# Optimization experiments

Measured on AMD Instinct MI355X. Metric: run time of the kernel, lower is better.

The kernel has to match this reference:

```python
import jax, jax.numpy as jnp
import numpy as np

N, D_IN = 65536, 512
H1, H2, D_SH = 1024, 1024, 512   # shared net: num_nodes_shared = [1024, 1024, 512]
HI = 512                          # indiv hidden width, num_nodes_indiv = [512, 512]


def setup_inputs() -> dict:
    key = jax.random.key(0)
    ks = jax.random.split(key, 16)
    s = 0.02
    inp = {
        "input": jax.random.normal(ks[0], (N, D_IN), jnp.float32),
        "treatment": jax.random.randint(ks[1], (N,), 0, 2, jnp.int32),
        # shared net (hidden ReLU layers + linear output, all with bias)
        "W0": jax.random.normal(ks[2], (D_IN, H1), jnp.float32) * s,
        "b0": jnp.zeros((H1,), jnp.float32),
        "W1": jax.random.normal(ks[3], (H1, H2), jnp.float32) * s,
        "b1": jnp.zeros((H2,), jnp.float32),
        "W2": jax.random.normal(ks[4], (H2, D_SH), jnp.float32) * s,
        "b2": jnp.zeros((D_SH,), jnp.float32),
        # risk net 0 (output layer has no bias)
        "A0": jax.random.normal(ks[5], (D_SH, HI), jnp.float32) * s,
        "a0": jnp.zeros((HI,), jnp.float32),
        "A1": jax.random.normal(ks[6], (HI, HI), jnp.float32) * s,
        "a1": jnp.zeros((HI,), jnp.float32),
        "A2": jax.random.normal(ks[7], (HI, 1), jnp.float32) * s,
        # risk net 1
        "C0": jax.random.normal(ks[8], (D_SH, HI), jnp.float32) * s,
        "c0": jnp.zeros((HI,), jnp.float32),
        "C1": jax.random.normal(ks[9], (HI, HI), jnp.float32) * s,
        "c1": jnp.zeros((HI,), jnp.float32),
        "C2": jax.random.normal(ks[10], (HI, 1), jnp.float32) * s,
    }
    return inp


def _risk_net(h, U0, u0, U1, u1, U2):
    h = jax.nn.relu(h @ U0 + u0)
    h = jax.nn.relu(h @ U1 + u1)
    return h @ U2  # [N, 1], no output bias


def reference(input, treatment, W0, b0, W1, b1, W2, b2,
              A0, a0, A1, a1, A2, C0, c0, C1, c1, C2):
    # shared MLP
    h = jax.nn.relu(input @ W0 + b0)
    h = jax.nn.relu(h @ W1 + b1)
    out = h @ W2 + b2                     # [N, D_SH]
    # Binary expert routing. The torch code gathers samples per treatment,
    # runs each group through its own MLP and scatters results back; the
    # math is equivalent to applying both experts and selecting per sample.
    y0 = _risk_net(out, A0, a0, A1, a1, A2)[:, 0]  # [N]
    y1 = _risk_net(out, C0, c0, C1, c1, C2)[:, 0]  # [N]
    y = jnp.where(treatment == 0, y0, y1)          # [N]
    return (y, out)
```

## Files before the change

kernel.cpp:

```cpp
#include <hip/hip_runtime.h>
#include <hip/hip_bf16.h>
#include <stdint.h>

typedef short short8 __attribute__((ext_vector_type(8)));
typedef float f32x4 __attribute__((ext_vector_type(4)));

#define NSAMP 65536
#define AS1 __attribute__((address_space(1)))
#define AS3 __attribute__((address_space(3)))

__device__ __forceinline__ unsigned short f2bf(float f) {
    union { float f; unsigned u; } v; v.f = f;
    unsigned u = v.u;
    u += 0x7fffu + ((u >> 16) & 1u);
    return (unsigned short)(u >> 16);
}


__global__ void k_convert_bf16(const float* __restrict__ in, unsigned short* __restrict__ out, int n8) {
    int i = blockIdx.x * blockDim.x + threadIdx.x;
    if (i >= n8) return;
    const float4* p = (const float4*)in + (size_t)i * 2;
    float4 a = p[0], b = p[1];
    short8 o;
    o[0] = (short)f2bf(a.x); o[1] = (short)f2bf(a.y);
    o[2] = (short)f2bf(a.z); o[3] = (short)f2bf(a.w);
    o[4] = (short)f2bf(b.x); o[5] = (short)f2bf(b.y);
    o[6] = (short)f2bf(b.z); o[7] = (short)f2bf(b.w);
    ((short8*)out)[i] = o;
}

struct PrepArgs {
    const float *W0, *W1, *W2, *A0, *C0, *A1, *C1, *a0v, *c0v;
    unsigned short *W0T, *W1T, *W2T, *RT0, *A1T, *C1T;
    float *bcat, *y0, *y1;
};
__global__ void k_prep(PrepArgs p) {
    int i = blockIdx.x * blockDim.x + threadIdx.x;
    if (i < 524288)  { int k = i >> 10, n = i & 1023; p.W0T[n * 512 + k] = f2bf(p.W0[i]); return; }
    i -= 524288;
    if (i < 1048576) { int k = i >> 10, n = i & 1023; p.W1T[n * 1024 + k] = f2bf(p.W1[i]); return; }
    i -= 1048576;
    if (i < 524288)  { int k = i >> 9, n = i & 511; p.W2T[n * 1024 + k] = f2bf(p.W2[i]); return; }
    i -= 524288;
    if (i < 262144)  { int k = i >> 9, n = i & 511; p.RT0[n * 512 + k] = f2bf(p.A0[i]); return; }
    i -= 262144;
    if (i < 262144)  { int k = i >> 9, n = i & 511; p.RT0[(512 + n) * 512 + k] = f2bf(p.C0[i]); return; }
    i -= 262144;
    if (i < 262144)  { int k = i >> 9, n = i & 511; p.A1T[n * 512 + k] = f2bf(p.A1[i]); return; }
    i -= 262144;
    if (i < 262144)  { int k = i >> 9, n = i & 511; p.C1T[n * 512 + k] = f2bf(p.C1[i]); return; }
    i -= 262144;
    if (i < 512)     { p.bcat[i] = p.a0v[i]; return; }
    i -= 512;
    if (i < 512)     { p.bcat[512 + i] = p.c0v[i]; return; }
    i -= 512;
    if (i < 65536)   { p.y0[i] = 0.f; return; }
    i -= 65536;
    if (i < 65536)   { p.y1[i] = 0.f; return; }
}

__global__ void k_select(const float* __restrict__ y0, const float* __restrict__ y1,
                         const int* __restrict__ t, float* __restrict__ y, int n) {
    int i = blockIdx.x * blockDim.x + threadIdx.x;
    if (i < n) y[i] = (t[i] == 0) ? y0[i] : y1[i];
}

template<int MODE>
__global__ __launch_bounds__(512, 2)
void k_gemm256(const unsigned short* __restrict__ A, int lda, int colOff,
               const unsigned short* __restrict__ BT,
               const float* __restrict__ bias,
               unsigned short* __restrict__ Cbf,
               float* __restrict__ Cf32,
               const float* __restrict__ w2,
               float* __restrict__ ydot,
               int Ncols, int K, int NB)
{
    __shared__ __align__(16) char lds[131072];

    const int tid  = threadIdx.x;
    const int lane = tid & 63;
    const int wid  = tid >> 6;
    const int wr   = wid >> 2;
    const int wcn  = wid & 3;

    const int nwg = gridDim.x;
    const int bid = blockIdx.x;
    const int swz = (bid & 7) * (nwg >> 3) + (bid >> 3);
    const int mt = swz / NB, nt = swz % NB;
    const int m0 = mt << 8, n0 = nt << 8;

    const int srow = tid >> 2;
    const int scs  = (tid & 3) ^ ((srow >> 1) & 3);
    const unsigned short* gA0 = A  + (size_t)(m0 + srow) * lda + colOff + scs * 8;
    const unsigned short* gA1 = gA0 + (size_t)128 * lda;
    const unsigned short* gB0 = BT + (size_t)(n0 + srow) * K + scs * 8;
    const unsigned short* gB1 = gB0 + (size_t)128 * K;
    const int ldst = wid * 1024;

#define STAGE_BLK(dbuf, blkoff, g0, g1, koff)                                            \
    do {                                                                                 \
        __builtin_amdgcn_global_load_lds((const AS1 void*)((g0) + (koff)),               \
                                         (AS3 void*)((dbuf) + (blkoff) + ldst), 16, 0, 0); \
        __builtin_amdgcn_global_load_lds((const AS1 void*)((g1) + (koff)),               \
                                         (AS3 void*)((dbuf) + (blkoff) + 8192 + ldst), 16, 0, 0); \
    } while (0)

    int aOff[8], bOff[4];
#pragma unroll
    for (int i = 0; i < 8; ++i) {
        int r = wr * 128 + i * 16 + (lane & 15);
        aOff[i] = r * 64 + ((((lane >> 4) ^ ((r >> 1) & 3))) << 4);
    }
#pragma unroll
    for (int j = 0; j < 4; ++j) {
        int r = wcn * 64 + j * 16 + (lane & 15);
        bOff[j] = r * 64 + ((((lane >> 4) ^ ((r >> 1) & 3))) << 4);
    }

    f32x4 acc[8][4];
#pragma unroll
    for (int i = 0; i < 8; ++i)
#pragma unroll
        for (int j = 0; j < 4; ++j) acc[i][j] = (f32x4)0.f;

    const int KT = K >> 6;

    STAGE_BLK(lds, 0,     gA0, gA1, 0);
    STAGE_BLK(lds, 32768, gB0, gB1, 0);
    STAGE_BLK(lds, 16384, gA0, gA1, 32);
    STAGE_BLK(lds, 49152, gB0, gB1, 32);
    asm volatile("s_waitcnt vmcnt(4)" ::: "memory");
    __builtin_amdgcn_s_barrier();

    for (int t = 0; t < KT; ++t) {
        const char* sbuf = lds + (t & 1) * 65536;
        char* dbuf = lds + ((t + 1) & 1) * 65536;
        const int koff = ((t + 1) << 6);
        const bool st = (t + 1 < KT);
        short8 af[4], bfv[4];

#pragma unroll
        for (int i = 0; i < 4; ++i) af[i]  = *(const short8*)(sbuf + aOff[i]);
#pragma unroll
        for (int j = 0; j < 4; ++j) bfv[j] = *(const short8*)(sbuf + 32768 + bOff[j]);
        if (st) STAGE_BLK(dbuf, 0, gA0, gA1, koff);
        __builtin_amdgcn_s_barrier();
        asm volatile("s_waitcnt lgkmcnt(0)" ::: "memory");
        __builtin_amdgcn_sched_barrier(0);
        __builtin_amdgcn_s_setprio(1);
#pragma unroll
        for (int i = 0; i < 4; ++i)
#pragma unroll
            for (int j = 0; j < 4; ++j)
                acc[i][j] = __builtin_amdgcn_mfma_f32_16x16x32_bf16(af[i], bfv[j], acc[i][j], 0, 0, 0);
        __builtin_amdgcn_s_setprio(0);
        __builtin_amdgcn_s_barrier();

#pragma unroll
        for (int i = 0; i < 4; ++i) af[i] = *(const short8*)(sbuf + aOff[4 + i]);
        if (st) STAGE_BLK(dbuf, 32768, gB0, gB1, koff);
        __builtin_amdgcn_s_barrier();
        asm volatile("s_waitcnt lgkmcnt(0)" ::: "memory");
        __builtin_amdgcn_sched_barrier(0);
        __builtin_amdgcn_s_setprio(1);
#pragma unroll
        for (int i = 0; i < 4; ++i)
#pragma unroll
            for (int j = 0; j < 4; ++j)
                acc[4 + i][j] = __builtin_amdgcn_mfma_f32_16x16x32_bf16(af[i], bfv[j], acc[4 + i][j], 0, 0, 0);
        __builtin_amdgcn_s_setprio(0);
        if (st) { asm volatile("s_waitcnt vmcnt(4)" ::: "memory"); }
        else    { asm volatile("s_waitcnt vmcnt(0)" ::: "memory"); }
        __builtin_amdgcn_sched_barrier(0);
        __builtin_amdgcn_s_barrier();

#pragma unroll
        for (int i = 0; i < 4; ++i) af[i]  = *(const short8*)(sbuf + 16384 + aOff[i]);
#pragma unroll
        for (int j = 0; j < 4; ++j) bfv[j] = *(const short8*)(sbuf + 49152 + bOff[j]);
        if (st) STAGE_BLK(dbuf, 16384, gA0, gA1, koff + 32);
        __builtin_amdgcn_s_barrier();
        asm volatile("s_waitcnt lgkmcnt(0)" ::: "memory");
        __builtin_amdgcn_sched_barrier(0);
        __builtin_amdgcn_s_setprio(1);
#pragma unroll
        for (int i = 0; i < 4; ++i)
#pragma unroll
            for (int j = 0; j < 4; ++j)
                acc[i][j] = __builtin_amdgcn_mfma_f32_16x16x32_bf16(af[i], bfv[j], acc[i][j], 0, 0, 0);
        __builtin_amdgcn_s_setprio(0);
        __builtin_amdgcn_s_barrier();

#pragma unroll
        for (int i = 0; i < 4; ++i) af[i] = *(const short8*)(sbuf + 16384 + aOff[4 + i]);
        if (st) STAGE_BLK(dbuf, 49152, gB0, gB1, koff + 32);
        __builtin_amdgcn_s_barrier();
        asm volatile("s_waitcnt lgkmcnt(0)" ::: "memory");
        __builtin_amdgcn_sched_barrier(0);
        __builtin_amdgcn_s_setprio(1);
#pragma unroll
        for (int i = 0; i < 4; ++i)
#pragma unroll
            for (int j = 0; j < 4; ++j)
                acc[4 + i][j] = __builtin_amdgcn_mfma_f32_16x16x32_bf16(af[i], bfv[j], acc[4 + i][j], 0, 0, 0);
        __builtin_amdgcn_s_setprio(0);
        if (st) { asm volatile("s_waitcnt vmcnt(4)" ::: "memory"); }
        __builtin_amdgcn_sched_barrier(0);
        __builtin_amdgcn_s_barrier();
    }
#undef STAGE_BLK

    const int mbase = m0 + wr * 128 + (lane >> 4) * 4;
    const int nbase = n0 + wcn * 64 + (lane & 15);

    if (MODE == 2) {
        float bv[4], wv[4];
#pragma unroll
        for (int j = 0; j < 4; ++j) {
            int ncol = nbase + j * 16;
            bv[j] = bias[ncol];
            wv[j] = w2[ncol];
        }
#pragma unroll
        for (int i = 0; i < 8; ++i) {
#pragma unroll
            for (int r = 0; r < 4; ++r) {
                float p = 0.f;
#pragma unroll
                for (int j = 0; j < 4; ++j) {
                    float v = fmaxf(acc[i][j][r] + bv[j], 0.f);
                    p += v * wv[j];
                }
                p += __shfl_xor(p, 1);
                p += __shfl_xor(p, 2);
                p += __shfl_xor(p, 4);
                p += __shfl_xor(p, 8);
                if ((lane & 15) == 0) {
                    atomicAdd(&ydot[mbase + i * 16 + r], p);
                }
            }
        }
    } else {
        float bv[4];
#pragma unroll
        for (int j = 0; j < 4; ++j) bv[j] = bias[nbase + j * 16];
#pragma unroll
        for (int i = 0; i < 8; ++i) {
#pragma unroll
            for (int j = 0; j < 4; ++j) {
                int ncol = nbase + j * 16;
#pragma unroll
                for (int r = 0; r < 4; ++r) {
                    float v = acc[i][j][r] + bv[j];
                    if (MODE == 0) v = fmaxf(v, 0.f);
                    size_t idx = (size_t)(mbase + i * 16 + r) * Ncols + ncol;
                    if (MODE == 1) Cf32[idx] = v;
                    Cbf[idx] = f2bf(v);
                }
            }
        }
    }
}


extern "C" void kernel_launch(void* const* d_in, const int* in_sizes, int n_in,
                              void* d_out, int out_size, void* d_ws, size_t ws_size,
                              hipStream_t stream) {
    const float* X  = (const float*)d_in[0];
    const int*  TR  = (const int*)d_in[1];
    const float* W0 = (const float*)d_in[2];  const float* b0 = (const float*)d_in[3];
    const float* W1 = (const float*)d_in[4];  const float* b1 = (const float*)d_in[5];
    const float* W2 = (const float*)d_in[6];  const float* b2 = (const float*)d_in[7];
    const float* A0 = (const float*)d_in[8];  const float* a0 = (const float*)d_in[9];
    const float* A1 = (const float*)d_in[10]; const float* a1 = (const float*)d_in[11];
    const float* A2 = (const float*)d_in[12];
    const float* C0 = (const float*)d_in[13]; const float* c0 = (const float*)d_in[14];
    const float* C1 = (const float*)d_in[15]; const float* c1 = (const float*)d_in[16];
    const float* C2 = (const float*)d_in[17];

    float* y_out   = (float*)d_out;
    float* out_out = (float*)d_out + NSAMP;

    char* ws = (char*)d_ws;
    size_t off = 0;
    auto alloc = [&](size_t bytes) -> char* {
        char* p = ws + off;
        off += (bytes + 255) & ~(size_t)255;
        return p;
    };
    unsigned short* Xb  = (unsigned short*)alloc((size_t)NSAMP * 512 * 2);
    unsigned short* H1b = (unsigned short*)alloc((size_t)NSAMP * 1024 * 2);
    unsigned short* H2b = (unsigned short*)alloc((size_t)NSAMP * 1024 * 2);
    unsigned short* OUTb = H1b;
    unsigned short* R01  = H2b;
    unsigned short* W0T = (unsigned short*)alloc(512 * 1024 * 2);
    unsigned short* W1T = (unsigned short*)alloc(1024 * 1024 * 2);
    unsigned short* W2T = (unsigned short*)alloc(1024 * 512 * 2);
    unsigned short* RT0 = (unsigned short*)alloc(1024 * 512 * 2);
    unsigned short* A1T = (unsigned short*)alloc(512 * 512 * 2);
    unsigned short* C1T = (unsigned short*)alloc(512 * 512 * 2);
    float* bcat = (float*)alloc(1024 * 4);
    float* y0 = (float*)alloc(NSAMP * 4);
    float* y1 = (float*)alloc(NSAMP * 4);

    k_convert_bf16<<<(NSAMP * 512 / 8 + 255) / 256, 256, 0, stream>>>(X, Xb, NSAMP * 512 / 8);
    PrepArgs pa;
    pa.W0 = W0; pa.W1 = W1; pa.W2 = W2; pa.A0 = A0; pa.C0 = C0; pa.A1 = A1; pa.C1 = C1;
    pa.a0v = a0; pa.c0v = c0;
    pa.W0T = W0T; pa.W1T = W1T; pa.W2T = W2T; pa.RT0 = RT0; pa.A1T = A1T; pa.C1T = C1T;
    pa.bcat = bcat; pa.y0 = y0; pa.y1 = y1;
    k_prep<<<(3277824 + 255) / 256, 256, 0, stream>>>(pa);

    const int MB = NSAMP / 256;

    k_gemm256<0><<<MB * 4, 512, 0, stream>>>(Xb, 512, 0, W0T, b0, H1b, nullptr, nullptr, nullptr, 1024, 512, 4);
    k_gemm256<0><<<MB * 4, 512, 0, stream>>>(H1b, 1024, 0, W1T, b1, H2b, nullptr, nullptr, nullptr, 1024, 1024, 4);
    k_gemm256<1><<<MB * 2, 512, 0, stream>>>(H2b, 1024, 0, W2T, b2, OUTb, out_out, nullptr, nullptr, 512, 1024, 2);

    k_gemm256<0><<<MB * 4, 512, 0, stream>>>(OUTb, 512, 0, RT0, bcat, R01, nullptr, nullptr, nullptr, 1024, 512, 4);

    k_gemm256<2><<<MB * 2, 512, 0, stream>>>(R01, 1024, 0,   A1T, a1, nullptr, nullptr, A2, y0, 512, 512, 2);
    k_gemm256<2><<<MB * 2, 512, 0, stream>>>(R01, 1024, 512, C1T, c1, nullptr, nullptr, C2, y1, 512, 512, 2);

    k_select<<<(NSAMP + 255) / 256, 256, 0, stream>>>(y0, y1, TR, y_out, NSAMP);
}
```

Before: 568.4 us.

## Make GEMM blocks own full row strips with cross-tile prefetch and fused expert select

Each GEMM workgroup now handles one 256-row strip and loops over every N tile, so the grid is exactly 256 blocks. The next tile's first K-slab is prefetched while the current tile finishes, and the accumulator is reset between tiles. The MFMA operands are swapped so each lane holds contiguous columns, which allows vectorized bias loads and packed 64-bit bf16 and f32x4 stores. The two expert MODE-2 launches are merged into one kernel that adds into y only for rows whose treatment matches the expert, which removes the select kernel and the y0/y1 buffers. The risk is lower parallelism per launch (one block per CU-ish) and the loss of the L2-friendly tile swizzle.

```diff
diff --git a/kernel.cpp b/kernel.cpp
--- a/kernel.cpp
+++ b/kernel.cpp
@@ -9,11 +9,11 @@
 #define AS1 __attribute__((address_space(1)))
 #define AS3 __attribute__((address_space(3)))
 
-__device__ __forceinline__ unsigned short f2bf(float f) {
+__device__ __forceinline__ unsigned f2bf(float f) {
     union { float f; unsigned u; } v; v.f = f;
     unsigned u = v.u;
     u += 0x7fffu + ((u >> 16) & 1u);
-    return (unsigned short)(u >> 16);
+    return u >> 16;
 }
 
 
@@ -33,7 +33,7 @@
 struct PrepArgs {
     const float *W0, *W1, *W2, *A0, *C0, *A1, *C1, *a0v, *c0v;
     unsigned short *W0T, *W1T, *W2T, *RT0, *A1T, *C1T;
-    float *bcat, *y0, *y1;
+    float *bcat, *yout;
 };
 __global__ void k_prep(PrepArgs p) {
     int i = blockIdx.x * blockDim.x + threadIdx.x;
@@ -55,27 +55,18 @@
     i -= 512;
     if (i < 512)     { p.bcat[512 + i] = p.c0v[i]; return; }
     i -= 512;
-    if (i < 65536)   { p.y0[i] = 0.f; return; }
-    i -= 65536;
-    if (i < 65536)   { p.y1[i] = 0.f; return; }
-}
-
-__global__ void k_select(const float* __restrict__ y0, const float* __restrict__ y1,
-                         const int* __restrict__ t, float* __restrict__ y, int n) {
-    int i = blockIdx.x * blockDim.x + threadIdx.x;
-    if (i < n) y[i] = (t[i] == 0) ? y0[i] : y1[i];
+    if (i < 65536)   { p.yout[i] = 0.f; return; }
 }
 
 template<int MODE>
 __global__ __launch_bounds__(512, 2)
-void k_gemm256(const unsigned short* __restrict__ A, int lda, int colOff,
-               const unsigned short* __restrict__ BT,
-               const float* __restrict__ bias,
-               unsigned short* __restrict__ Cbf,
-               float* __restrict__ Cf32,
-               const float* __restrict__ w2,
-               float* __restrict__ ydot,
-               int Ncols, int K, int NB)
+void k_gemm256(const unsigned short* __restrict__ A, int lda,
+               const unsigned short* __restrict__ BT, const unsigned short* __restrict__ BT2,
+               const float* __restrict__ bias, const float* __restrict__ bias2,
+               unsigned short* __restrict__ Cbf, float* __restrict__ Cf32,
+               const float* __restrict__ w2, const float* __restrict__ w2b,
+               const int* __restrict__ TRt, float* __restrict__ ydot,
+               int Ncols, int K, int TPB)
 {
     __shared__ __align__(16) char lds[131072];
 
@@ -84,20 +75,28 @@
     const int wid  = tid >> 6;
     const int wr   = wid >> 2;
     const int wcn  = wid & 3;
-
-    const int nwg = gridDim.x;
-    const int bid = blockIdx.x;
-    const int swz = (bid & 7) * (nwg >> 3) + (bid >> 3);
-    const int mt = swz / NB, nt = swz % NB;
-    const int m0 = mt << 8, n0 = nt << 8;
+    const int m0   = blockIdx.x << 8;
 
     const int srow = tid >> 2;
     const int scs  = (tid & 3) ^ ((srow >> 1) & 3);
-    const unsigned short* gA0 = A  + (size_t)(m0 + srow) * lda + colOff + scs * 8;
-    const unsigned short* gA1 = gA0 + (size_t)128 * lda;
-    const unsigned short* gB0 = BT + (size_t)(n0 + srow) * K + scs * 8;
-    const unsigned short* gB1 = gB0 + (size_t)128 * K;
     const int ldst = wid * 1024;
+
+    auto mk = [&](int tau, const unsigned short*& a0, const unsigned short*& a1,
+                  const unsigned short*& b0, const unsigned short*& b1) {
+        int cOff = 0;
+        int n0e = tau << 8;
+        const unsigned short* Bsel = BT;
+        if (MODE == 2) {
+            int expert = tau >> 1;
+            n0e = (tau & 1) << 8;
+            cOff = expert << 9;
+            if (expert) Bsel = BT2;
+        }
+        a0 = A + (size_t)(m0 + srow) * lda + cOff + scs * 8;
+        a1 = a0 + (size_t)128 * lda;
+        b0 = Bsel + (size_t)(n0e + srow) * K + scs * 8;
+        b1 = b0 + (size_t)128 * K;
+    };
 
 #define STAGE_BLK(dbuf, blkoff, g0, g1, koff)                                            \
     do {                                                                                 \
@@ -125,143 +124,164 @@
 #pragma unroll
         for (int j = 0; j < 4; ++j) acc[i][j] = (f32x4)0.f;
 
-    const int KT = K >> 6;
-
-    STAGE_BLK(lds, 0,     gA0, gA1, 0);
-    STAGE_BLK(lds, 32768, gB0, gB1, 0);
-    STAGE_BLK(lds, 16384, gA0, gA1, 32);
-    STAGE_BLK(lds, 49152, gB0, gB1, 32);
+    const int KT  = K >> 6;
+    const int TOT = TPB * KT;
+
+    const unsigned short *cA0, *cA1, *cB0, *cB1;
+    mk(0, cA0, cA1, cB0, cB1);
+    const unsigned short *nA0 = cA0, *nA1 = cA1, *nB0 = cB0, *nB1 = cB1;
+
+    STAGE_BLK(lds, 0,     cA0, cA1, 0);
+    STAGE_BLK(lds, 32768, cB0, cB1, 0);
+    STAGE_BLK(lds, 16384, cA0, cA1, 32);
+    STAGE_BLK(lds, 49152, cB0, cB1, 32);
     asm volatile("s_waitcnt vmcnt(4)" ::: "memory");
     __builtin_amdgcn_s_barrier();
 
-    for (int t = 0; t < KT; ++t) {
-        const char* sbuf = lds + (t & 1) * 65536;
-        char* dbuf = lds + ((t + 1) & 1) * 65536;
-        const int koff = ((t + 1) << 6);
-        const bool st = (t + 1 < KT);
-        short8 af[4], bfv[4];
-
-#pragma unroll
-        for (int i = 0; i < 4; ++i) af[i]  = *(const short8*)(sbuf + aOff[i]);
-#pragma unroll
-        for (int j = 0; j < 4; ++j) bfv[j] = *(const short8*)(sbuf + 32768 + bOff[j]);
-        if (st) STAGE_BLK(dbuf, 0, gA0, gA1, koff);
-        __builtin_amdgcn_s_barrier();
-        asm volatile("s_waitcnt lgkmcnt(0)" ::: "memory");
-        __builtin_amdgcn_sched_barrier(0);
-        __builtin_amdgcn_s_setprio(1);
-#pragma unroll
-        for (int i = 0; i < 4; ++i)
-#pragma unroll
-            for (int j = 0; j < 4; ++j)
-                acc[i][j] = __builtin_amdgcn_mfma_f32_16x16x32_bf16(af[i], bfv[j], acc[i][j], 0, 0, 0);
-        __builtin_amdgcn_s_setprio(0);
-        __builtin_amdgcn_s_barrier();
-
-#pragma unroll
-        for (int i = 0; i < 4; ++i) af[i] = *(const short8*)(sbuf + aOff[4 + i]);
-        if (st) STAGE_BLK(dbuf, 32768, gB0, gB1, koff);
-        __builtin_amdgcn_s_barrier();
-        asm volatile("s_waitcnt lgkmcnt(0)" ::: "memory");
-        __builtin_amdgcn_sched_barrier(0);
-        __builtin_amdgcn_s_setprio(1);
-#pragma unroll
-        for (int i = 0; i < 4; ++i)
-#pragma unroll
-            for (int j = 0; j < 4; ++j)
-                acc[4 + i][j] = __builtin_amdgcn_mfma_f32_16x16x32_bf16(af[i], bfv[j], acc[4 + i][j], 0, 0, 0);
-        __builtin_amdgcn_s_setprio(0);
-        if (st) { asm volatile("s_waitcnt vmcnt(4)" ::: "memory"); }
-        else    { asm volatile("s_waitcnt vmcnt(0)" ::: "memory"); }
-        __builtin_amdgcn_sched_barrier(0);
-        __builtin_amdgcn_s_barrier();
-
-#pragma unroll
-        for (int i = 0; i < 4; ++i) af[i]  = *(const short8*)(sbuf + 16384 + aOff[i]);
-#pragma unroll
-        for (int j = 0; j < 4; ++j) bfv[j] = *(const short8*)(sbuf + 49152 + bOff[j]);
-        if (st) STAGE_BLK(dbuf, 16384, gA0, gA1, koff + 32);
-        __builtin_amdgcn_s_barrier();
-        asm volatile("s_waitcnt lgkmcnt(0)" ::: "memory");
-        __builtin_amdgcn_sched_barrier(0);
-        __builtin_amdgcn_s_setprio(1);
-#pragma unroll
-        for (int i = 0; i < 4; ++i)
-#pragma unroll
-            for (int j = 0; j < 4; ++j)
-                acc[i][j] = __builtin_amdgcn_mfma_f32_16x16x32_bf16(af[i], bfv[j], acc[i][j], 0, 0, 0);
-        __builtin_amdgcn_s_setprio(0);
-        __builtin_amdgcn_s_barrier();
-
-#pragma unroll
-        for (int i = 0; i < 4; ++i) af[i] = *(const short8*)(sbuf + 16384 + aOff[4 + i]);
-        if (st) STAGE_BLK(dbuf, 49152, gB0, gB1, koff + 32);
-        __builtin_amdgcn_s_barrier();
-        asm volatile("s_waitcnt lgkmcnt(0)" ::: "memory");
-        __builtin_amdgcn_sched_barrier(0);
-        __builtin_amdgcn_s_setprio(1);
-#pragma unroll
-        for (int i = 0; i < 4; ++i)
-#pragma unroll
-            for (int j = 0; j < 4; ++j)
-                acc[4 + i][j] = __builtin_amdgcn_mfma_f32_16x16x32_bf16(af[i], bfv[j], acc[4 + i][j], 0, 0, 0);
-        __builtin_amdgcn_s_setprio(0);
-        if (st) { asm volatile("s_waitcnt vmcnt(4)" ::: "memory"); }
-        __builtin_amdgcn_sched_barrier(0);
-        __builtin_amdgcn_s_barrier();
-    }
-#undef STAGE_BLK
-
-    const int mbase = m0 + wr * 128 + (lane >> 4) * 4;
-    const int nbase = n0 + wcn * 64 + (lane & 15);
-
-    if (MODE == 2) {
-        float bv[4], wv[4];
-#pragma unroll
-        for (int j = 0; j < 4; ++j) {
-            int ncol = nbase + j * 16;
-            bv[j] = bias[ncol];
-            wv[j] = w2[ncol];
+    int g = 0;
+    for (int tau = 0; tau < TPB; ++tau) {
+        if (tau + 1 < TPB) mk(tau + 1, nA0, nA1, nB0, nB1);
+
+        for (int t = 0; t < KT; ++t, ++g) {
+            const char* sbuf = lds + (g & 1) * 65536;
+            char* dbuf = lds + ((g + 1) & 1) * 65536;
+            const bool inTile = (t + 1 < KT);
+            const bool st = (g + 1 < TOT);
+            const unsigned short* sA0 = inTile ? cA0 : nA0;
+            const unsigned short* sA1 = inTile ? cA1 : nA1;
+            const unsigned short* sB0 = inTile ? cB0 : nB0;
+            const unsigned short* sB1 = inTile ? cB1 : nB1;
+            const int koff = inTile ? ((t + 1) << 6) : 0;
+            short8 af[4], bfv[4];
+
+#pragma unroll
+            for (int i = 0; i < 4; ++i) af[i]  = *(const short8*)(sbuf + aOff[i]);
+#pragma unroll
+            for (int j = 0; j < 4; ++j) bfv[j] = *(const short8*)(sbuf + 32768 + bOff[j]);
+            if (st) STAGE_BLK(dbuf, 0, sA0, sA1, koff);
+            __builtin_amdgcn_s_barrier();
+            asm volatile("s_waitcnt lgkmcnt(0)" ::: "memory");
+            __builtin_amdgcn_sched_barrier(0);
+            __builtin_amdgcn_s_setprio(1);
+#pragma unroll
+            for (int i = 0; i < 4; ++i)
+#pragma unroll
+                for (int j = 0; j < 4; ++j)
+                    acc[i][j] = __builtin_amdgcn_mfma_f32_16x16x32_bf16(bfv[j], af[i], acc[i][j], 0, 0, 0);
+            __builtin_amdgcn_s_setprio(0);
+            __builtin_amdgcn_s_barrier();
+
+#pragma unroll
+            for (int i = 0; i < 4; ++i) af[i] = *(const short8*)(sbuf + aOff[4 + i]);
+            if (st) STAGE_BLK(dbuf, 32768, sB0, sB1, koff);
+            __builtin_amdgcn_s_barrier();
+            asm volatile("s_waitcnt lgkmcnt(0)" ::: "memory");
+            __builtin_amdgcn_sched_barrier(0);
+            __builtin_amdgcn_s_setprio(1);
+#pragma unroll
+            for (int i = 0; i < 4; ++i)
+#pragma unroll
+                for (int j = 0; j < 4; ++j)
+                    acc[4 + i][j] = __builtin_amdgcn_mfma_f32_16x16x32_bf16(bfv[j], af[i], acc[4 + i][j], 0, 0, 0);
+            __builtin_amdgcn_s_setprio(0);
+            if (st) { asm volatile("s_waitcnt vmcnt(4)" ::: "memory"); }
+            else    { asm volatile("s_waitcnt vmcnt(0)" ::: "memory"); }
+            __builtin_amdgcn_sched_barrier(0);
+            __builtin_amdgcn_s_barrier();
+
+#pragma unroll
+            for (int i = 0; i < 4; ++i) af[i]  = *(const short8*)(sbuf + 16384 + aOff[i]);
+#pragma unroll
+            for (int j = 0; j < 4; ++j) bfv[j] = *(const short8*)(sbuf + 49152 + bOff[j]);
+            if (st) STAGE_BLK(dbuf, 16384, sA0, sA1, koff + 32);
+            __builtin_amdgcn_s_barrier();
+            asm volatile("s_waitcnt lgkmcnt(0)" ::: "memory");
+            __builtin_amdgcn_sched_barrier(0);
+            __builtin_amdgcn_s_setprio(1);
+#pragma unroll
+            for (int i = 0; i < 4; ++i)
+#pragma unroll
+                for (int j = 0; j < 4; ++j)
+                    acc[i][j] = __builtin_amdgcn_mfma_f32_16x16x32_bf16(bfv[j], af[i], acc[i][j], 0, 0, 0);
+            __builtin_amdgcn_s_setprio(0);
+            __builtin_amdgcn_s_barrier();
+
+#pragma unroll
+            for (int i = 0; i < 4; ++i) af[i] = *(const short8*)(sbuf + 16384 + aOff[4 + i]);
+            if (st) STAGE_BLK(dbuf, 49152, sB0, sB1, koff + 32);
+            __builtin_amdgcn_s_barrier();
+            asm volatile("s_waitcnt lgkmcnt(0)" ::: "memory");
+            __builtin_amdgcn_sched_barrier(0);
+            __builtin_amdgcn_s_setprio(1);
+#pragma unroll
+            for (int i = 0; i < 4; ++i)
+#pragma unroll
+                for (int j = 0; j < 4; ++j)
+                    acc[4 + i][j] = __builtin_amdgcn_mfma_f32_16x16x32_bf16(bfv[j], af[i], acc[4 + i][j], 0, 0, 0);
+            __builtin_amdgcn_s_setprio(0);
+            if (st) { asm volatile("s_waitcnt vmcnt(4)" ::: "memory"); }
+            __builtin_amdgcn_sched_barrier(0);
+            __builtin_amdgcn_s_barrier();
         }
-#pragma unroll
-        for (int i = 0; i < 8; ++i) {
-#pragma unroll
-            for (int r = 0; r < 4; ++r) {
+
+        if (MODE == 2) {
+            const int expert = tau >> 1;
+            const int n0e = (tau & 1) << 8;
+            const float* be = expert ? bias2 : bias;
+            const float* we = expert ? w2b : w2;
+            const int nb = n0e + wcn * 64 + ((lane >> 4) << 2);
+            f32x4 bv[4], wv[4];
+#pragma unroll
+            for (int j = 0; j < 4; ++j) {
+                bv[j] = *(const f32x4*)(be + nb + j * 16);
+                wv[j] = *(const f32x4*)(we + nb + j * 16);
+            }
+#pragma unroll
+            for (int i = 0; i < 8; ++i) {
                 float p = 0.f;
 #pragma unroll
+                for (int j = 0; j < 4; ++j)
+#pragma unroll
+                    for (int r = 0; r < 4; ++r)
+                        p += fmaxf(acc[i][j][r] + bv[j][r], 0.f) * wv[j][r];
+                p += __shfl_xor(p, 16);
+                p += __shfl_xor(p, 32);
+                const int m = m0 + wr * 128 + i * 16 + (lane & 15);
+                if (lane < 16 && TRt[m] == expert) atomicAdd(&ydot[m], p);
+            }
+        } else {
+            const int n0e = tau << 8;
+            const int nb = n0e + wcn * 64 + ((lane >> 4) << 2);
+            f32x4 bv[4];
+#pragma unroll
+            for (int j = 0; j < 4; ++j) bv[j] = *(const f32x4*)(bias + nb + j * 16);
+#pragma unroll
+            for (int i = 0; i < 8; ++i) {
+                const int m = m0 + wr * 128 + i * 16 + (lane & 15);
+                unsigned short* pb = Cbf + (size_t)m * Ncols + nb;
+#pragma unroll
                 for (int j = 0; j < 4; ++j) {
-                    float v = fmaxf(acc[i][j][r] + bv[j], 0.f);
-                    p += v * wv[j];
-                }
-                p += __shfl_xor(p, 1);
-                p += __shfl_xor(p, 2);
-                p += __shfl_xor(p, 4);
-                p += __shfl_xor(p, 8);
-                if ((lane & 15) == 0) {
-                    atomicAdd(&ydot[mbase + i * 16 + r], p);
+                    f32x4 v = acc[i][j] + bv[j];
+                    if (MODE == 0) {
+#pragma unroll
+                        for (int r = 0; r < 4; ++r) v[r] = fmaxf(v[r], 0.f);
+                    }
+                    if (MODE == 1) *(f32x4*)(Cf32 + (size_t)m * Ncols + nb + j * 16) = v;
+                    unsigned long long pk =
+                        (unsigned long long)(f2bf(v[0]) | (f2bf(v[1]) << 16)) |
+                        ((unsigned long long)(f2bf(v[2]) | (f2bf(v[3]) << 16)) << 32);
+                    *(unsigned long long*)(pb + j * 16) = pk;
                 }
             }
         }
-    } else {
-        float bv[4];
-#pragma unroll
-        for (int j = 0; j < 4; ++j) bv[j] = bias[nbase + j * 16];
-#pragma unroll
-        for (int i = 0; i < 8; ++i) {
-#pragma unroll
-            for (int j = 0; j < 4; ++j) {
-                int ncol = nbase + j * 16;
-#pragma unroll
-                for (int r = 0; r < 4; ++r) {
-                    float v = acc[i][j][r] + bv[j];
-                    if (MODE == 0) v = fmaxf(v, 0.f);
-                    size_t idx = (size_t)(mbase + i * 16 + r) * Ncols + ncol;
-                    if (MODE == 1) Cf32[idx] = v;
-                    Cbf[idx] = f2bf(v);
-                }
-            }
-        }
+
+#pragma unroll
+        for (int i = 0; i < 8; ++i)
+#pragma unroll
+            for (int j = 0; j < 4; ++j) acc[i][j] = (f32x4)0.f;
+        cA0 = nA0; cA1 = nA1; cB0 = nB0; cB1 = nB1;
     }
+#undef STAGE_BLK
 }
 
 
@@ -302,27 +322,30 @@
     unsigned short* A1T = (unsigned short*)alloc(512 * 512 * 2);
     unsigned short* C1T = (unsigned short*)alloc(512 * 512 * 2);
     float* bcat = (float*)alloc(1024 * 4);
-    float* y0 = (float*)alloc(NSAMP * 4);
-    float* y1 = (float*)alloc(NSAMP * 4);
 
     k_convert_bf16<<<(NSAMP * 512 / 8 + 255) / 256, 256, 0, stream>>>(X, Xb, NSAMP * 512 / 8);
     PrepArgs pa;
     pa.W0 = W0; pa.W1 = W1; pa.W2 = W2; pa.A0 = A0; pa.C0 = C0; pa.A1 = A1; pa.C1 = C1;
     pa.a0v = a0; pa.c0v = c0;
     pa.W0T = W0T; pa.W1T = W1T; pa.W2T = W2T; pa.RT0 = RT0; pa.A1T = A1T; pa.C1T = C1T;
-    pa.bcat = bcat; pa.y0 = y0; pa.y1 = y1;
-    k_prep<<<(3277824 + 255) / 256, 256, 0, stream>>>(pa);
-
-    const int MB = NSAMP / 256;
-
-    k_gemm256<0><<<MB * 4, 512, 0, stream>>>(Xb, 512, 0, W0T, b0, H1b, nullptr, nullptr, nullptr, 1024, 512, 4);
-    k_gemm256<0><<<MB * 4, 512, 0, stream>>>(H1b, 1024, 0, W1T, b1, H2b, nullptr, nullptr, nullptr, 1024, 1024, 4);
-    k_gemm256<1><<<MB * 2, 512, 0, stream>>>(H2b, 1024, 0, W2T, b2, OUTb, out_out, nullptr, nullptr, 512, 1024, 2);
-
-    k_gemm256<0><<<MB * 4, 512, 0, stream>>>(OUTb, 512, 0, RT0, bcat, R01, nullptr, nullptr, nullptr, 1024, 512, 4);
-
-    k_gemm256<2><<<MB * 2, 512, 0, stream>>>(R01, 1024, 0,   A1T, a1, nullptr, nullptr, A2, y0, 512, 512, 2);
-    k_gemm256<2><<<MB * 2, 512, 0, stream>>>(R01, 1024, 512, C1T, c1, nullptr, nullptr, C2, y1, 512, 512, 2);
-
-    k_select<<<(NSAMP + 255) / 256, 256, 0, stream>>>(y0, y1, TR, y_out, NSAMP);
-}
+    pa.bcat = bcat; pa.yout = y_out;
+    k_prep<<<(3212288 + 255) / 256, 256, 0, stream>>>(pa);
+
+    k_gemm256<0><<<256, 512, 0, stream>>>(Xb, 512, W0T, nullptr, b0, nullptr,
+                                          H1b, nullptr, nullptr, nullptr, nullptr, nullptr,
+                                          1024, 512, 4);
+    k_gemm256<0><<<256, 512, 0, stream>>>(H1b, 1024, W1T, nullptr, b1, nullptr,
+                                          H2b, nullptr, nullptr, nullptr, nullptr, nullptr,
+                                          1024, 1024, 4);
+    k_gemm256<1><<<256, 512, 0, stream>>>(H2b, 1024, W2T, nullptr, b2, nullptr,
+                                          OUTb, out_out, nullptr, nullptr, nullptr, nullptr,
+                                          512, 1024, 2);
+
+    k_gemm256<0><<<256, 512, 0, stream>>>(OUTb, 512, RT0, nullptr, bcat, nullptr,
+                                          R01, nullptr, nullptr, nullptr, nullptr, nullptr,
+                                          1024, 512, 4);
+
+    k_gemm256<2><<<256, 512, 0, stream>>>(R01, 1024, A1T, C1T, a1, c1,
+                                          nullptr, nullptr, A2, C2, TR, y_out,
+                                          512, 512, 4);
+}
```

Measured after the change: 622.7 us. 1.1x slower.
